# Performance work log

Hardware: AMD Instinct MI355X
Metric: run time of the kernel (lower is better)

Reference implementation:

```python
import jax, jax.numpy as jnp
import numpy as np

B, C, H, W = 32, 2, 224, 224
P = 4096   # mask points per instance
N = 256    # HV_NUM_OF_HYPOTHESES


def setup_inputs() -> dict:
    key = jax.random.key(0)
    k1, k2, k3 = jax.random.split(key, 3)
    uv_img = jax.random.normal(k1, (B, C, H, W), dtype=jnp.float32)
    pts = jax.random.randint(k2, (B, P, 2), 0, H, dtype=jnp.int64 if jax.config.read('jax_enable_x64') else jnp.int32)
    pair_idx = jax.random.randint(k3, (B, N, 2), 0, P, dtype=pts.dtype)
    return {"uv_img": uv_img, "pts": pts, "pair_idx": pair_idx}


def _per_instance(uv, p, pi):
    # uv: [2,H,W], p: [P,2] int, pi: [N,2] int
    pt0 = p[pi[:, 0]]                      # [N,2] (row, col)
    pt1 = p[pi[:, 1]]                      # [N,2]
    # uv values at each sampled point: uv_img[:, row, col] -> [N,2]
    uv0 = uv[:, pt0[:, 0], pt0[:, 1]].T    # [N,2]
    uv1 = uv[:, pt1[:, 0], pt1[:, 1]].T    # [N,2]
    pt0f = pt0.astype(uv.dtype)
    pt1f = pt1.astype(uv.dtype)
    # A = [uv0 | -uv1], B = pt1 - pt0 (2x2 pinverse solve per hypothesis)
    A = jnp.stack([uv0, -uv1], axis=-1)    # [N,2,2]
    Bv = (pt1f - pt0f)[..., None]          # [N,2,1]
    X = jnp.matmul(jnp.linalg.pinv(A), Bv) # [N,2,1]
    Y = X[:, 0, :] * uv0 + pt0f            # [N,2] hypotheses (row, col)
    # hypothesis weights: count of mask points whose uv direction agrees
    pts_uv = uv[:, p[:, 0], p[:, 1]].T     # [P,2]
    a = Y[:, None, :] - p[None, :, :].astype(uv.dtype)      # [N,P,2]
    a = a / jnp.linalg.norm(a, axis=-1, keepdims=True)
    agree = jnp.einsum('npk,pk->np', a, pts_uv) > 0          # [N,P]
    w = jnp.sum(agree, axis=-1).astype(uv.dtype)             # [N]
    weighted_mean = jnp.sum(Y * w[:, None], axis=0) / jnp.sum(w)
    return weighted_mean[::-1]             # pixel_xy = (col, row)


def reference(uv_img, pts, pair_idx):
    # filled_pixel_xy: [B, 2]
    return jax.vmap(_per_instance)(uv_img, pts, pair_idx)
```

## Files before the change

kernel.cpp:

```cpp
#include <hip/hip_runtime.h>
#include <hip/hip_fp16.h>

#define BATCH 32
#define CH    2
#define HH    224
#define WW    224
#define PP    4096
#define NN    256
#define SPLIT 32
#define TILE  (PP / SPLIT)
#define TILE2 (TILE / 2)

#define WS_Y_OFF    0
#define WS_PART_OFF (64 * 1024)
#define WS_NEED     (96 * 1024)

struct alignas(16) PtPack { __half2 u, v, nc, pad; };

__device__ inline float2 solve_pair(const float* __restrict__ uvb,
                                    const int* __restrict__ ptsb,
                                    const int* __restrict__ pairb, int n)
{
    const int2 pr = *(const int2*)(pairb + n * 2);
    const int2 p0 = *(const int2*)(ptsb + pr.x * 2);
    const int2 p1 = *(const int2*)(ptsb + pr.y * 2);
    const int y0 = p0.x, x0 = p0.y;
    const int y1 = p1.x, x1 = p1.y;

    const float u0a = uvb[y0 * WW + x0];
    const float u0b = uvb[HH * WW + y0 * WW + x0];
    const float u1a = uvb[y1 * WW + x1];
    const float u1b = uvb[HH * WW + y1 * WW + x1];

    const double a00 = (double)u0a, a01 = -(double)u1a;
    const double a10 = (double)u0b, a11 = -(double)u1b;
    const double b0 = (double)(y1 - y0), b1 = (double)(x1 - x0);
    const double det = a00 * a11 - a01 * a10;
    const double frob2 = a00 * a00 + a01 * a01 + a10 * a10 + a11 * a11;

    double t0;
    if (fabs(det) > 1e-12 * frob2) {
        t0 = (b0 * a11 - b1 * a01) / det;
    } else if (frob2 > 0.0) {
        t0 = (a00 * b0 + a10 * b1) / frob2;
    } else {
        t0 = 0.0;
    }
    return make_float2((float)(t0 * (double)u0a + (double)y0),
                       (float)(t0 * (double)u0b + (double)x0));
}

__global__ __launch_bounds__(256)
void hough_solve(const float* __restrict__ uv,
                 const int* __restrict__ pts,
                 const int* __restrict__ pair,
                 float2* __restrict__ yv)
{
    const int b = blockIdx.x;
    const int t = threadIdx.x;
    const float* uvb = uv + (size_t)b * CH * HH * WW;
    yv[b * NN + t] = solve_pair(uvb, pts + b * PP * 2, pair + b * NN * 2, t);
}

__global__ __launch_bounds__(256, 4)
void hough_vote(const float* __restrict__ uv,
                const int* __restrict__ pts,
                const float2* __restrict__ yv,
                double* __restrict__ part)
{
    const int blk = blockIdx.x;
    const int b = blk / SPLIT;
    const int s = blk % SPLIT;
    const int t = threadIdx.x;

    const float* uvb = uv + (size_t)b * CH * HH * WW;
    const int* ptsb = pts + b * PP * 2;

    __shared__ PtPack tile[TILE2];
    if (t < TILE2) {
        const int p = s * TILE + 2 * t;
        const int4 pp = *(const int4*)(ptsb + p * 2);
        const float u0 = uvb[pp.x * WW + pp.y];
        const float v0 = uvb[HH * WW + pp.x * WW + pp.y];
        const float u1 = uvb[pp.z * WW + pp.w];
        const float v1 = uvb[HH * WW + pp.z * WW + pp.w];
        const float c0 = (float)pp.x * u0 + (float)pp.y * v0;
        const float c1 = (float)pp.z * u1 + (float)pp.w * v1;
        PtPack pk;
        pk.u  = __floats2half2_rn(u0, u1);
        pk.v  = __floats2half2_rn(v0, v1);
        pk.nc = __floats2half2_rn(-c0, -c1);
        pk.pad = __floats2half2_rn(0.0f, 0.0f);
        tile[t] = pk;
    }

    const float2 Yn = yv[b * NN + t];
    const float yy = Yn.x, yx = Yn.y;
    const float maxab = fmaxf(fabsf(yy), fabsf(yx));
    const float sc = (maxab > 1024.0f) ? (1024.0f / maxab) : 1.0f;
    const __half2 yy2 = __float2half2_rn(yy * sc);
    const __half2 yx2 = __float2half2_rn(yx * sc);
    const __half2 sc2 = __float2half2_rn(sc);

    __syncthreads();

    unsigned negs = 0u;
    #pragma unroll 4
    for (int j = 0; j < TILE2; ++j) {
        const PtPack q = tile[j];
        __half2 d = __hmul2(yy2, q.u);
        d = __hfma2(yx2, q.v, d);
        d = __hfma2(sc2, q.nc, d);
        unsigned ub;
        __builtin_memcpy(&ub, &d, 4);
        negs += (ub >> 15) & 0x00010001u;
    }
    const int cw = TILE - (int)(negs & 0xFFFFu) - (int)(negs >> 16);

    double wy = (double)cw * (double)yy;
    double wx = (double)cw * (double)yx;
    double ww = (double)cw;
    #pragma unroll
    for (int off = 32; off > 0; off >>= 1) {
        wy += __shfl_down(wy, off);
        wx += __shfl_down(wx, off);
        ww += __shfl_down(ww, off);
    }

    __shared__ double red[4 * 3];
    const int wid = t >> 6;
    if ((t & 63) == 0) {
        red[wid * 3 + 0] = wy;
        red[wid * 3 + 1] = wx;
        red[wid * 3 + 2] = ww;
    }
    __syncthreads();
    if (t == 0) {
        double* o = part + (size_t)blk * 4;
        o[0] = red[0] + red[3] + red[6] + red[9];
        o[1] = red[1] + red[4] + red[7] + red[10];
        o[2] = red[2] + red[5] + red[8] + red[11];
    }
}

__global__ __launch_bounds__(256)
void hough_final(const double* __restrict__ part, float* __restrict__ out)
{
    const int t = threadIdx.x;
    const int bb = t >> 3;
    const int l8 = t & 7;
    double sy = 0.0, sx = 0.0, sw = 0.0;
    #pragma unroll
    for (int k = l8; k < SPLIT; k += 8) {
        const double* o = part + (size_t)(bb * SPLIT + k) * 4;
        sy += o[0];
        sx += o[1];
        sw += o[2];
    }
    #pragma unroll
    for (int off = 1; off < 8; off <<= 1) {
        sy += __shfl_xor(sy, off);
        sx += __shfl_xor(sx, off);
        sw += __shfl_xor(sw, off);
    }
    if (l8 == 0) {
        out[bb * 2 + 0] = (float)(sx / sw);
        out[bb * 2 + 1] = (float)(sy / sw);
    }
}

__global__ __launch_bounds__(256, 4)
void hough_partial_fb(const float* __restrict__ uv,
                      const int* __restrict__ pts,
                      const int* __restrict__ pair,
                      double* __restrict__ part)
{
    const int blk = blockIdx.x;
    const int b = blk / SPLIT;
    const int s = blk % SPLIT;
    const int t = threadIdx.x;

    const float* uvb = uv + (size_t)b * CH * HH * WW;
    const int* ptsb = pts + b * PP * 2;

    __shared__ PtPack tile[TILE2];
    if (t < TILE2) {
        const int p = s * TILE + 2 * t;
        const int4 pp = *(const int4*)(ptsb + p * 2);
        const float u0 = uvb[pp.x * WW + pp.y];
        const float v0 = uvb[HH * WW + pp.x * WW + pp.y];
        const float u1 = uvb[pp.z * WW + pp.w];
        const float v1 = uvb[HH * WW + pp.z * WW + pp.w];
        const float c0 = (float)pp.x * u0 + (float)pp.y * v0;
        const float c1 = (float)pp.z * u1 + (float)pp.w * v1;
        PtPack pk;
        pk.u  = __floats2half2_rn(u0, u1);
        pk.v  = __floats2half2_rn(v0, v1);
        pk.nc = __floats2half2_rn(-c0, -c1);
        pk.pad = __floats2half2_rn(0.0f, 0.0f);
        tile[t] = pk;
    }

    const float2 Yn = solve_pair(uvb, ptsb, pair + b * NN * 2, t);
    const float yy = Yn.x, yx = Yn.y;
    const float maxab = fmaxf(fabsf(yy), fabsf(yx));
    const float sc = (maxab > 1024.0f) ? (1024.0f / maxab) : 1.0f;
    const __half2 yy2 = __float2half2_rn(yy * sc);
    const __half2 yx2 = __float2half2_rn(yx * sc);
    const __half2 sc2 = __float2half2_rn(sc);

    __syncthreads();

    unsigned negs = 0u;
    #pragma unroll 4
    for (int j = 0; j < TILE2; ++j) {
        const PtPack q = tile[j];
        __half2 d = __hmul2(yy2, q.u);
        d = __hfma2(yx2, q.v, d);
        d = __hfma2(sc2, q.nc, d);
        unsigned ub;
        __builtin_memcpy(&ub, &d, 4);
        negs += (ub >> 15) & 0x00010001u;
    }
    const int cw = TILE - (int)(negs & 0xFFFFu) - (int)(negs >> 16);

    double wy = (double)cw * (double)yy;
    double wx = (double)cw * (double)yx;
    double ww = (double)cw;
    #pragma unroll
    for (int off = 32; off > 0; off >>= 1) {
        wy += __shfl_down(wy, off);
        wx += __shfl_down(wx, off);
        ww += __shfl_down(ww, off);
    }
    __shared__ double red[4 * 3];
    const int wid = t >> 6;
    if ((t & 63) == 0) {
        red[wid * 3 + 0] = wy;
        red[wid * 3 + 1] = wx;
        red[wid * 3 + 2] = ww;
    }
    __syncthreads();
    if (t == 0) {
        double* o = part + (size_t)blk * 4;
        o[0] = red[0] + red[3] + red[6] + red[9];
        o[1] = red[1] + red[4] + red[7] + red[10];
        o[2] = red[2] + red[5] + red[8] + red[11];
    }
}

extern "C" void kernel_launch(void* const* d_in, const int* in_sizes, int n_in,
                              void* d_out, int out_size, void* d_ws, size_t ws_size,
                              hipStream_t stream)
{
    const float* uv   = (const float*)d_in[0];
    const int*   pts  = (const int*)d_in[1];
    const int*   pair = (const int*)d_in[2];
    float* out = (float*)d_out;
    char* ws = (char*)d_ws;

    if (ws_size >= WS_NEED) {
        float2* yv   = (float2*)(ws + WS_Y_OFF);
        double* part = (double*)(ws + WS_PART_OFF);
        hough_solve<<<BATCH, 256, 0, stream>>>(uv, pts, pair, yv);
        hough_vote<<<BATCH * SPLIT, 256, 0, stream>>>(uv, pts, yv, part);
        hough_final<<<1, 256, 0, stream>>>(part, out);
    } else {
        double* part = (double*)ws;
        hough_partial_fb<<<BATCH * SPLIT, 256, 0, stream>>>(uv, pts, pair, part);
        hough_final<<<1, 256, 0, stream>>>(part, out);
    }
}
```

Before: 20.38 us.

## Fuse final reduction into vote kernel via last-block atomic counter

Removes the separate final-reduction launch. Each vote block publishes its partial sums and increments a per-batch counter, and the last block to arrive for a batch reduces all partials and writes the output. The split count is halved so there are fewer, longer blocks. The solve kernel is re-gridded into 128 blocks of 64 threads and also resets the counters. This saves one kernel launch at the cost of atomic and fence overhead, with less parallelism in the vote phase. The fallback path now also uses the solve kernel, which writes into workspace it may not have enough room for.

```diff
diff --git a/kernel.cpp b/kernel.cpp
--- a/kernel.cpp
+++ b/kernel.cpp
@@ -7,13 +7,15 @@
 #define WW    224
 #define PP    4096
 #define NN    256
-#define SPLIT 32
+#define SPLIT 16
 #define TILE  (PP / SPLIT)
 #define TILE2 (TILE / 2)
 
 #define WS_Y_OFF    0
 #define WS_PART_OFF (64 * 1024)
-#define WS_NEED     (96 * 1024)
+#define WS_CNT_OFF  (80 * 1024)
+#define WS_NEED     (84 * 1024)
+#define CNT_STRIDE  32
 
 struct alignas(16) PtPack { __half2 u, v, nc, pad; };
 
@@ -50,23 +52,30 @@
                        (float)(t0 * (double)u0b + (double)x0));
 }
 
-__global__ __launch_bounds__(256)
+__global__ __launch_bounds__(64)
 void hough_solve(const float* __restrict__ uv,
                  const int* __restrict__ pts,
                  const int* __restrict__ pair,
-                 float2* __restrict__ yv)
-{
-    const int b = blockIdx.x;
-    const int t = threadIdx.x;
+                 float2* __restrict__ yv,
+                 unsigned* __restrict__ cnt)
+{
+    const int blk = blockIdx.x;
+    const int b = blk >> 2;
+    const int n = ((blk & 3) << 6) + threadIdx.x;
     const float* uvb = uv + (size_t)b * CH * HH * WW;
-    yv[b * NN + t] = solve_pair(uvb, pts + b * PP * 2, pair + b * NN * 2, t);
+    yv[b * NN + n] = solve_pair(uvb, pts + b * PP * 2, pair + b * NN * 2, n);
+    if (blk == 0 && threadIdx.x < BATCH)
+        __hip_atomic_store(&cnt[threadIdx.x * CNT_STRIDE], 0u,
+                           __ATOMIC_RELAXED, __HIP_MEMORY_SCOPE_AGENT);
 }
 
 __global__ __launch_bounds__(256, 4)
 void hough_vote(const float* __restrict__ uv,
                 const int* __restrict__ pts,
                 const float2* __restrict__ yv,
-                double* __restrict__ part)
+                double* __restrict__ part,
+                unsigned* __restrict__ cnt,
+                float* __restrict__ out)
 {
     const int blk = blockIdx.x;
     const int b = blk / SPLIT;
@@ -105,7 +114,7 @@
     __syncthreads();
 
     unsigned negs = 0u;
-    #pragma unroll 4
+    #pragma unroll 8
     for (int j = 0; j < TILE2; ++j) {
         const PtPack q = tile[j];
         __half2 d = __hmul2(yy2, q.u);
@@ -128,6 +137,7 @@
     }
 
     __shared__ double red[4 * 3];
+    __shared__ int lastFlag;
     const int wid = t >> 6;
     if ((t & 63) == 0) {
         red[wid * 3 + 0] = wy;
@@ -137,43 +147,45 @@
     __syncthreads();
     if (t == 0) {
         double* o = part + (size_t)blk * 4;
-        o[0] = red[0] + red[3] + red[6] + red[9];
-        o[1] = red[1] + red[4] + red[7] + red[10];
-        o[2] = red[2] + red[5] + red[8] + red[11];
-    }
-}
-
-__global__ __launch_bounds__(256)
-void hough_final(const double* __restrict__ part, float* __restrict__ out)
-{
-    const int t = threadIdx.x;
-    const int bb = t >> 3;
-    const int l8 = t & 7;
-    double sy = 0.0, sx = 0.0, sw = 0.0;
-    #pragma unroll
-    for (int k = l8; k < SPLIT; k += 8) {
-        const double* o = part + (size_t)(bb * SPLIT + k) * 4;
-        sy += o[0];
-        sx += o[1];
-        sw += o[2];
-    }
-    #pragma unroll
-    for (int off = 1; off < 8; off <<= 1) {
-        sy += __shfl_xor(sy, off);
-        sx += __shfl_xor(sx, off);
-        sw += __shfl_xor(sw, off);
-    }
-    if (l8 == 0) {
-        out[bb * 2 + 0] = (float)(sx / sw);
-        out[bb * 2 + 1] = (float)(sy / sw);
+        __hip_atomic_store(&o[0], red[0] + red[3] + red[6] + red[9],
+                           __ATOMIC_RELAXED, __HIP_MEMORY_SCOPE_AGENT);
+        __hip_atomic_store(&o[1], red[1] + red[4] + red[7] + red[10],
+                           __ATOMIC_RELAXED, __HIP_MEMORY_SCOPE_AGENT);
+        __hip_atomic_store(&o[2], red[2] + red[5] + red[8] + red[11],
+                           __ATOMIC_RELAXED, __HIP_MEMORY_SCOPE_AGENT);
+        const unsigned prev = __hip_atomic_fetch_add(
+            &cnt[b * CNT_STRIDE], 1u, __ATOMIC_RELEASE,
+            __HIP_MEMORY_SCOPE_AGENT);
+        lastFlag = (prev == SPLIT - 1);
+    }
+    __syncthreads();
+
+    if (lastFlag && t < SPLIT) {
+        if (t == 0)
+            (void)__hip_atomic_load(&cnt[b * CNT_STRIDE],
+                                    __ATOMIC_ACQUIRE, __HIP_MEMORY_SCOPE_AGENT);
+        const double* o = part + (size_t)(b * SPLIT + t) * 4;
+        double sy = __hip_atomic_load(&o[0], __ATOMIC_RELAXED, __HIP_MEMORY_SCOPE_AGENT);
+        double sx = __hip_atomic_load(&o[1], __ATOMIC_RELAXED, __HIP_MEMORY_SCOPE_AGENT);
+        double sw = __hip_atomic_load(&o[2], __ATOMIC_RELAXED, __HIP_MEMORY_SCOPE_AGENT);
+        #pragma unroll
+        for (int off = 1; off < SPLIT; off <<= 1) {
+            sy += __shfl_xor(sy, off, SPLIT);
+            sx += __shfl_xor(sx, off, SPLIT);
+            sw += __shfl_xor(sw, off, SPLIT);
+        }
+        if (t == 0) {
+            out[b * 2 + 0] = (float)(sx / sw);
+            out[b * 2 + 1] = (float)(sy / sw);
+        }
     }
 }
 
 __global__ __launch_bounds__(256, 4)
-void hough_partial_fb(const float* __restrict__ uv,
-                      const int* __restrict__ pts,
-                      const int* __restrict__ pair,
-                      double* __restrict__ part)
+void hough_vote_nb(const float* __restrict__ uv,
+                   const int* __restrict__ pts,
+                   const float2* __restrict__ yv,
+                   double* __restrict__ part)
 {
     const int blk = blockIdx.x;
     const int b = blk / SPLIT;
@@ -201,7 +213,7 @@
         tile[t] = pk;
     }
 
-    const float2 Yn = solve_pair(uvb, ptsb, pair + b * NN * 2, t);
+    const float2 Yn = yv[b * NN + t];
     const float yy = Yn.x, yx = Yn.y;
     const float maxab = fmaxf(fabsf(yy), fabsf(yx));
     const float sc = (maxab > 1024.0f) ? (1024.0f / maxab) : 1.0f;
@@ -212,7 +224,7 @@
     __syncthreads();
 
     unsigned negs = 0u;
-    #pragma unroll 4
+    #pragma unroll 8
     for (int j = 0; j < TILE2; ++j) {
         const PtPack q = tile[j];
         __half2 d = __hmul2(yy2, q.u);
@@ -249,6 +261,32 @@
     }
 }
 
+__global__ __launch_bounds__(256)
+void hough_final(const double* __restrict__ part, float* __restrict__ out)
+{
+    const int t = threadIdx.x;
+    const int bb = t >> 3;
+    const int l8 = t & 7;
+    double sy = 0.0, sx = 0.0, sw = 0.0;
+    #pragma unroll
+    for (int k = l8; k < SPLIT; k += 8) {
+        const double* o = part + (size_t)(bb * SPLIT + k) * 4;
+        sy += o[0];
+        sx += o[1];
+        sw += o[2];
+    }
+    #pragma unroll
+    for (int off = 1; off < 8; off <<= 1) {
+        sy += __shfl_xor(sy, off);
+        sx += __shfl_xor(sx, off);
+        sw += __shfl_xor(sw, off);
+    }
+    if (l8 == 0) {
+        out[bb * 2 + 0] = (float)(sx / sw);
+        out[bb * 2 + 1] = (float)(sy / sw);
+    }
+}
+
 extern "C" void kernel_launch(void* const* d_in, const int* in_sizes, int n_in,
                               void* d_out, int out_size, void* d_ws, size_t ws_size,
                               hipStream_t stream)
@@ -259,15 +297,16 @@
     float* out = (float*)d_out;
     char* ws = (char*)d_ws;
 
+    float2*   yv   = (float2*)(ws + WS_Y_OFF);
+    double*   part = (double*)(ws + WS_PART_OFF);
+    unsigned* cnt  = (unsigned*)(ws + WS_CNT_OFF);
+
     if (ws_size >= WS_NEED) {
-        float2* yv   = (float2*)(ws + WS_Y_OFF);
-        double* part = (double*)(ws + WS_PART_OFF);
-        hough_solve<<<BATCH, 256, 0, stream>>>(uv, pts, pair, yv);
-        hough_vote<<<BATCH * SPLIT, 256, 0, stream>>>(uv, pts, yv, part);
+        hough_solve<<<128, 64, 0, stream>>>(uv, pts, pair, yv, cnt);
+        hough_vote<<<BATCH * SPLIT, 256, 0, stream>>>(uv, pts, yv, part, cnt, out);
+    } else {
+        hough_solve<<<128, 64, 0, stream>>>(uv, pts, pair, yv, cnt);
+        hough_vote_nb<<<BATCH * SPLIT, 256, 0, stream>>>(uv, pts, yv, part);
         hough_final<<<1, 256, 0, stream>>>(part, out);
-    } else {
-        double* part = (double*)ws;
-        hough_partial_fb<<<BATCH * SPLIT, 256, 0, stream>>>(uv, pts, pair, part);
-        hough_final<<<1, 256, 0, stream>>>(part, out);
-    }
-}
+    }
+}
```

Result: slower. 22.41 us (+10.0%).

## Halve vote split, stage tile with all threads, spread solve over more blocks

Applied to the files above, without the earlier changes.

The vote kernel now splits each instance's points into 16 chunks instead of 32. Each block processes 256 points, and all 256 threads gather and pack one point each into shared memory as half-precision fields. The inner vote loop is unrolled 16 instead of 4. The solve kernel is relaunched as 128 blocks of 64 threads so it spreads across more CUs. Together these cut block count and partial-sum traffic and raise per-block work, at the cost of fewer blocks in flight for the vote kernel and scalar 2-byte shared stores during staging.

```diff
diff --git a/kernel.cpp b/kernel.cpp
--- a/kernel.cpp
+++ b/kernel.cpp
@@ -7,13 +7,13 @@
 #define WW    224
 #define PP    4096
 #define NN    256
-#define SPLIT 32
+#define SPLIT 16
 #define TILE  (PP / SPLIT)
 #define TILE2 (TILE / 2)
 
 #define WS_Y_OFF    0
 #define WS_PART_OFF (64 * 1024)
-#define WS_NEED     (96 * 1024)
+#define WS_NEED     (80 * 1024)
 
 struct alignas(16) PtPack { __half2 u, v, nc, pad; };
 
@@ -50,16 +50,17 @@
                        (float)(t0 * (double)u0b + (double)x0));
 }
 
-__global__ __launch_bounds__(256)
+__global__ __launch_bounds__(64)
 void hough_solve(const float* __restrict__ uv,
                  const int* __restrict__ pts,
                  const int* __restrict__ pair,
                  float2* __restrict__ yv)
 {
-    const int b = blockIdx.x;
-    const int t = threadIdx.x;
+    const int blk = blockIdx.x;
+    const int b = blk >> 2;
+    const int n = ((blk & 3) << 6) + threadIdx.x;
     const float* uvb = uv + (size_t)b * CH * HH * WW;
-    yv[b * NN + t] = solve_pair(uvb, pts + b * PP * 2, pair + b * NN * 2, t);
+    yv[b * NN + n] = solve_pair(uvb, pts + b * PP * 2, pair + b * NN * 2, n);
 }
 
 __global__ __launch_bounds__(256, 4)
@@ -77,21 +78,17 @@
     const int* ptsb = pts + b * PP * 2;
 
     __shared__ PtPack tile[TILE2];
-    if (t < TILE2) {
-        const int p = s * TILE + 2 * t;
-        const int4 pp = *(const int4*)(ptsb + p * 2);
-        const float u0 = uvb[pp.x * WW + pp.y];
-        const float v0 = uvb[HH * WW + pp.x * WW + pp.y];
-        const float u1 = uvb[pp.z * WW + pp.w];
-        const float v1 = uvb[HH * WW + pp.z * WW + pp.w];
-        const float c0 = (float)pp.x * u0 + (float)pp.y * v0;
-        const float c1 = (float)pp.z * u1 + (float)pp.w * v1;
-        PtPack pk;
-        pk.u  = __floats2half2_rn(u0, u1);
-        pk.v  = __floats2half2_rn(v0, v1);
-        pk.nc = __floats2half2_rn(-c0, -c1);
-        pk.pad = __floats2half2_rn(0.0f, 0.0f);
-        tile[t] = pk;
+    {
+        const int p = s * TILE + t;
+        const int2 pyx = *(const int2*)(ptsb + p * 2);
+        const float u = uvb[pyx.x * WW + pyx.y];
+        const float v = uvb[HH * WW + pyx.x * WW + pyx.y];
+        const float c = (float)pyx.x * u + (float)pyx.y * v;
+        __half* base = (__half*)&tile[t >> 1];
+        const int e = t & 1;
+        base[0 + e] = __float2half_rn(u);
+        base[2 + e] = __float2half_rn(v);
+        base[4 + e] = __float2half_rn(-c);
     }
 
     const float2 Yn = yv[b * NN + t];
@@ -105,7 +102,7 @@
     __syncthreads();
 
     unsigned negs = 0u;
-    #pragma unroll 4
+    #pragma unroll 16
     for (int j = 0; j < TILE2; ++j) {
         const PtPack q = tile[j];
         __half2 d = __hmul2(yy2, q.u);
@@ -184,21 +181,17 @@
     const int* ptsb = pts + b * PP * 2;
 
     __shared__ PtPack tile[TILE2];
-    if (t < TILE2) {
-        const int p = s * TILE + 2 * t;
-        const int4 pp = *(const int4*)(ptsb + p * 2);
-        const float u0 = uvb[pp.x * WW + pp.y];
-        const float v0 = uvb[HH * WW + pp.x * WW + pp.y];
-        const float u1 = uvb[pp.z * WW + pp.w];
-        const float v1 = uvb[HH * WW + pp.z * WW + pp.w];
-        const float c0 = (float)pp.x * u0 + (float)pp.y * v0;
-        const float c1 = (float)pp.z * u1 + (float)pp.w * v1;
-        PtPack pk;
-        pk.u  = __floats2half2_rn(u0, u1);
-        pk.v  = __floats2half2_rn(v0, v1);
-        pk.nc = __floats2half2_rn(-c0, -c1);
-        pk.pad = __floats2half2_rn(0.0f, 0.0f);
-        tile[t] = pk;
+    {
+        const int p = s * TILE + t;
+        const int2 pyx = *(const int2*)(ptsb + p * 2);
+        const float u = uvb[pyx.x * WW + pyx.y];
+        const float v = uvb[HH * WW + pyx.x * WW + pyx.y];
+        const float c = (float)pyx.x * u + (float)pyx.y * v;
+        __half* base = (__half*)&tile[t >> 1];
+        const int e = t & 1;
+        base[0 + e] = __float2half_rn(u);
+        base[2 + e] = __float2half_rn(v);
+        base[4 + e] = __float2half_rn(-c);
     }
 
     const float2 Yn = solve_pair(uvb, ptsb, pair + b * NN * 2, t);
@@ -212,7 +205,7 @@
     __syncthreads();
 
     unsigned negs = 0u;
-    #pragma unroll 4
+    #pragma unroll 16
     for (int j = 0; j < TILE2; ++j) {
         const PtPack q = tile[j];
         __half2 d = __hmul2(yy2, q.u);
@@ -262,7 +255,7 @@
     if (ws_size >= WS_NEED) {
         float2* yv   = (float2*)(ws + WS_Y_OFF);
         double* part = (double*)(ws + WS_PART_OFF);
-        hough_solve<<<BATCH, 256, 0, stream>>>(uv, pts, pair, yv);
+        hough_solve<<<128, 64, 0, stream>>>(uv, pts, pair, yv);
         hough_vote<<<BATCH * SPLIT, 256, 0, stream>>>(uv, pts, yv, part);
         hough_final<<<1, 256, 0, stream>>>(part, out);
     } else {
```

Result: faster. 19.91 us (-2.3%).
